# Optimization experiments

Measured on AMD Instinct MI355X. Metric: run time of the kernel, lower is better.

Reference implementation:

```python
import jax, jax.numpy as jnp
import numpy as np

N_NODES = 200000
N_EDGES = 3200000
NX = 8
NK = 2


def _l2norm(x, eps=1e-12):
    # F.normalize(x, p=2, dim=-1)
    n = jnp.linalg.norm(x, axis=-1, keepdims=True)
    return x / jnp.maximum(n, eps)


def _aniso_conv(x, src, dst, Kw, n_nodes):
    """For each kernel j: out_j[t] = sum_{e: dst[e]=t} Kw[j,e] * x[src[e]].
    Concatenate over kernels along the feature axis."""
    g = x[src]  # [E, d] gather
    def agg(w):  # w: [E]
        return jax.ops.segment_sum(w[:, None] * g, dst, num_segments=n_nodes)
    out = jax.vmap(agg)(Kw)  # [nk, N, d]
    return jnp.transpose(out, (1, 0, 2)).reshape(n_nodes, -1)  # [N, nk*d]


def setup_inputs() -> dict:
    key = jax.random.key(0)
    ks = jax.random.split(key, 8)
    x = jax.random.normal(ks[0], (N_NODES, NX), dtype=jnp.float32)
    src = jax.random.randint(ks[1], (N_EDGES,), 0, N_NODES, dtype=jnp.int64 if jax.config.jax_enable_x64 else jnp.int32)
    dst = jax.random.randint(ks[2], (N_EDGES,), 0, N_NODES, dtype=src.dtype)
    edge_index = jnp.stack([src, dst], axis=0)
    Kw = jax.random.normal(ks[3], (NK, N_EDGES), dtype=jnp.float32)
    d0, d1 = NX * NK, NX * NK * 2          # 16, 32
    d2 = d1 * NK                            # 64
    hidden, out_ch = 128, 64
    W0 = jax.random.normal(ks[4], (d0, d1), dtype=jnp.float32) / np.sqrt(d0)
    b0 = jnp.zeros((d1,), dtype=jnp.float32)
    W1 = jax.random.normal(ks[5], (d2, hidden), dtype=jnp.float32) / np.sqrt(d2)
    b1 = jnp.zeros((hidden,), dtype=jnp.float32)
    W2 = jax.random.normal(ks[6], (hidden, out_ch), dtype=jnp.float32) / np.sqrt(hidden)
    b2 = jnp.zeros((out_ch,), dtype=jnp.float32)
    return {"x": x, "edge_index": edge_index, "Kw": Kw,
            "W0": W0, "b0": b0, "W1": W1, "b1": b1, "W2": W2, "b2": b2}


def reference(x, edge_index, Kw, W0, b0, W1, b1, W2, b2):
    src, dst = edge_index[0], edge_index[1]
    n = x.shape[0]
    # layer 0: AnisoConv -> single-linear MLP -> L2 normalize
    h = _aniso_conv(x, src, dst, Kw, n)      # [N, 16]
    h = h @ W0 + b0                           # [N, 32]
    h = _l2norm(h)
    # layer 1: AnisoConv -> 2-layer MLP (ReLU between) -> L2 normalize
    h = _aniso_conv(h, src, dst, Kw, n)      # [N, 64]
    h = jax.nn.relu(h @ W1 + b1)             # [N, 128]
    h = h @ W2 + b2                           # [N, 64]
    h = _l2norm(h)
    return h
```

## Files before the change

kernel.cpp:

```cpp
#include <hip/hip_runtime.h>

#define NN 200000
#define NE 3200000
#define NB_SCAN 782
#define NBUCK 196
#define BSHIFT 10
#define BMASK 1023
#define SRCMASK 0x3FFFFu
#define NBLK_A 512
#define EPB (NE / NBLK_A)
#define NT_MLP1 12500

using bf16x8 = __attribute__((ext_vector_type(8))) short;
using f32x4  = __attribute__((ext_vector_type(4))) float;

__device__ __forceinline__ float bflo(unsigned u) { return __uint_as_float(u << 16); }
__device__ __forceinline__ float bfhi(unsigned u) { return __uint_as_float(u & 0xffff0000u); }
__device__ __forceinline__ unsigned short f2bfu(float f) {
  unsigned u = __float_as_uint(f);
  return (unsigned short)((u + 0x7fffu + ((u >> 16) & 1u)) >> 16);
}
__device__ __forceinline__ unsigned pack2(float a, float b) {
  return (unsigned)f2bfu(a) | ((unsigned)f2bfu(b) << 16);
}


__global__ __launch_bounds__(256) void bhist_kernel(const int* __restrict__ dst,
                                                    int* __restrict__ bhT) {
  __shared__ int h[NBUCK];
  for (int k = threadIdx.x; k < NBUCK; k += 256) h[k] = 0;
  __syncthreads();
  int base = blockIdx.x * EPB;
  for (int i = threadIdx.x; i < EPB; i += 256)
    atomicAdd(&h[dst[base + i] >> BSHIFT], 1);
  __syncthreads();
  for (int k = threadIdx.x; k < NBUCK; k += 256)
    bhT[k * NBLK_A + blockIdx.x] = h[k];
}

__global__ __launch_bounds__(NBLK_A) void bscan_kernel(int* __restrict__ bhT,
                                                       int* __restrict__ btot) {
  __shared__ int s[NBLK_A];
  int b = blockIdx.x;
  int v = bhT[b * NBLK_A + threadIdx.x];
  s[threadIdx.x] = v;
  __syncthreads();
#pragma unroll
  for (int off = 1; off < NBLK_A; off <<= 1) {
    int t = (threadIdx.x >= off) ? s[threadIdx.x - off] : 0;
    __syncthreads();
    s[threadIdx.x] += t;
    __syncthreads();
  }
  bhT[b * NBLK_A + threadIdx.x] = s[threadIdx.x] - v;
  if (threadIdx.x == NBLK_A - 1) btot[b] = s[NBLK_A - 1];
}

__global__ __launch_bounds__(256) void bbase_kernel(const int* __restrict__ btot,
                                                    int* __restrict__ bbase) {
  __shared__ int s[256];
  int v = (threadIdx.x < NBUCK) ? btot[threadIdx.x] : 0;
  s[threadIdx.x] = v;
  __syncthreads();
#pragma unroll
  for (int off = 1; off < 256; off <<= 1) {
    int t = (threadIdx.x >= off) ? s[threadIdx.x - off] : 0;
    __syncthreads();
    s[threadIdx.x] += t;
    __syncthreads();
  }
  if (threadIdx.x < NBUCK) bbase[threadIdx.x] = s[threadIdx.x] - v;
  if (threadIdx.x == NBUCK - 1) bbase[NBUCK] = s[threadIdx.x];
}

__global__ __launch_bounds__(256) void bplace_kernel(
    const int* __restrict__ src, const int* __restrict__ dst,
    const float* __restrict__ kw, const int* __restrict__ bhT,
    const int* __restrict__ bbase, uint2* __restrict__ bsorted) {
  __shared__ int cur[NBUCK];
  for (int k = threadIdx.x; k < NBUCK; k += 256)
    cur[k] = bbase[k] + bhT[k * NBLK_A + blockIdx.x];
  __syncthreads();
  int base = blockIdx.x * EPB;
  for (int i = threadIdx.x; i < EPB; i += 256) {
    int e = base + i;
    int d = dst[e];
    int p = atomicAdd(&cur[d >> BSHIFT], 1);
    uint2 u;
    u.x = (unsigned)src[e] | ((unsigned)(d & BMASK) << 18);
    u.y = pack2(kw[e], kw[NE + e]);
    bsorted[p] = u;
  }
}


__global__ __launch_bounds__(1024) void nhist_kernel(const uint2* __restrict__ bsorted,
                                                     const int* __restrict__ bbase,
                                                     int* __restrict__ cnt) {
  __shared__ int h[1024];
  h[threadIdx.x] = 0;
  __syncthreads();
  int b = blockIdx.x;
  int r0 = bbase[b], r1 = bbase[b + 1];
  for (int i = r0 + threadIdx.x; i < r1; i += 1024)
    atomicAdd(&h[bsorted[i].x >> 18], 1);
  __syncthreads();
  int node = b * 1024 + threadIdx.x;
  if (node < NN) cnt[node] = h[threadIdx.x];
}

__global__ __launch_bounds__(256) void scan1_kernel(const int* __restrict__ cnt,
                                                    int* __restrict__ offs,
                                                    int* __restrict__ bsums) {
  __shared__ int s[256];
  int i = blockIdx.x * 256 + threadIdx.x;
  int v = (i < NN) ? cnt[i] : 0;
  s[threadIdx.x] = v;
  __syncthreads();
#pragma unroll
  for (int off = 1; off < 256; off <<= 1) {
    int t = (threadIdx.x >= off) ? s[threadIdx.x - off] : 0;
    __syncthreads();
    s[threadIdx.x] += t;
    __syncthreads();
  }
  if (i < NN) offs[i] = s[threadIdx.x];
  if (threadIdx.x == 255) bsums[blockIdx.x] = s[255];
}

__global__ __launch_bounds__(1024) void scan2_kernel(int* __restrict__ bsums, int nb) {
  __shared__ int s[1024];
  int v = (threadIdx.x < nb) ? bsums[threadIdx.x] : 0;
  s[threadIdx.x] = v;
  __syncthreads();
#pragma unroll
  for (int off = 1; off < 1024; off <<= 1) {
    int t = (threadIdx.x >= off) ? s[threadIdx.x - off] : 0;
    __syncthreads();
    s[threadIdx.x] += t;
    __syncthreads();
  }
  if (threadIdx.x < nb) bsums[threadIdx.x] = s[threadIdx.x] - v;
}

__global__ __launch_bounds__(256) void scan3_kernel(const int* __restrict__ cnt,
                                                    const int* __restrict__ bsums,
                                                    int* __restrict__ offs) {
  int i = blockIdx.x * 256 + threadIdx.x;
  if (i >= NN) return;
  offs[i] = offs[i] - cnt[i] + bsums[blockIdx.x];
}

__global__ __launch_bounds__(1024) void nplace_kernel(const uint2* __restrict__ bsorted,
                                                      const int* __restrict__ bbase,
                                                      const int* __restrict__ offs,
                                                      uint2* __restrict__ sedge) {
  __shared__ int cur[1024];
  int b = blockIdx.x;
  int node = b * 1024 + threadIdx.x;
  cur[threadIdx.x] = (node < NN) ? offs[node] : 0;
  __syncthreads();
  int r0 = bbase[b], r1 = bbase[b + 1];
  for (int i = r0 + threadIdx.x; i < r1; i += 1024) {
    uint2 u = bsorted[i];
    int p = atomicAdd(&cur[u.x >> 18], 1);
    u.x &= SRCMASK;
    sedge[p] = u;
  }
}


__global__ __launch_bounds__(256) void fused0_kernel(
    const float* __restrict__ x, const int* __restrict__ offs,
    const int* __restrict__ cnt, const uint2* __restrict__ sedge,
    const float* __restrict__ W0, const float* __restrict__ b0,
    unsigned short* __restrict__ h1bf) {
  __shared__ float w0t[32][16];
  __shared__ float b0s[32];
  int tid = threadIdx.x;
  for (int i = tid; i < 16 * 32; i += 256) {
    int k = i >> 5, j = i & 31;
    w0t[j][k] = W0[i];
  }
  if (tid < 32) b0s[tid] = b0[tid];
  __syncthreads();

  int idx = blockIdx.x * 256 + tid;
  int node = idx >> 1, q = idx & 1;
  if (node >= NN) return;

  int start = offs[node];
  int deg = cnt[node];
  float a0 = 0.f, a1 = 0.f, a2 = 0.f, a3 = 0.f;
  float c0 = 0.f, c1 = 0.f, c2 = 0.f, c3 = 0.f;

  for (int i = 0; i < deg; ++i) {
    uint2 e = sedge[start + i];
    float k0 = bflo(e.y), k1 = bfhi(e.y);
    float4 v = *reinterpret_cast<const float4*>(x + (size_t)e.x * 8 + q * 4);
    a0 += k0 * v.x; a1 += k0 * v.y; a2 += k0 * v.z; a3 += k0 * v.w;
    c0 += k1 * v.x; c1 += k1 * v.y; c2 += k1 * v.z; c3 += k1 * v.w;
  }

  float pa0 = __shfl_xor(a0, 1), pa1 = __shfl_xor(a1, 1);
  float pa2 = __shfl_xor(a2, 1), pa3 = __shfl_xor(a3, 1);
  float pc0 = __shfl_xor(c0, 1), pc1 = __shfl_xor(c1, 1);
  float pc2 = __shfl_xor(c2, 1), pc3 = __shfl_xor(c3, 1);
  bool q0 = (q == 0);
  float h0 = q0 ? a0 : pa0, h1 = q0 ? a1 : pa1;
  float h2 = q0 ? a2 : pa2, h3 = q0 ? a3 : pa3;
  float h4 = q0 ? pa0 : a0, h5 = q0 ? pa1 : a1;
  float h6 = q0 ? pa2 : a2, h7 = q0 ? pa3 : a3;
  float h8 = q0 ? c0 : pc0, h9 = q0 ? c1 : pc1;
  float h10 = q0 ? c2 : pc2, h11 = q0 ? c3 : pc3;
  float h12 = q0 ? pc0 : c0, h13 = q0 ? pc1 : c1;
  float h14 = q0 ? pc2 : c2, h15 = q0 ? pc3 : c3;

  float o[16];
  float ss = 0.f;
#pragma unroll
  for (int jj = 0; jj < 16; ++jj) {
    int j = q * 16 + jj;
    float acc = b0s[j];
    acc += h0 * w0t[j][0] + h1 * w0t[j][1] + h2 * w0t[j][2] + h3 * w0t[j][3];
    acc += h4 * w0t[j][4] + h5 * w0t[j][5] + h6 * w0t[j][6] + h7 * w0t[j][7];
    acc += h8 * w0t[j][8] + h9 * w0t[j][9] + h10 * w0t[j][10] + h11 * w0t[j][11];
    acc += h12 * w0t[j][12] + h13 * w0t[j][13] + h14 * w0t[j][14] + h15 * w0t[j][15];
    o[jj] = acc;
    ss += acc * acc;
  }
  ss += __shfl_xor(ss, 1);
  float inv = 1.f / fmaxf(sqrtf(ss), 1e-12f);

  uint4* op = reinterpret_cast<uint4*>(h1bf + (size_t)node * 32 + q * 16);
  uint4 u0, u1;
  u0.x = pack2(o[0] * inv, o[1] * inv);  u0.y = pack2(o[2] * inv, o[3] * inv);
  u0.z = pack2(o[4] * inv, o[5] * inv);  u0.w = pack2(o[6] * inv, o[7] * inv);
  u1.x = pack2(o[8] * inv, o[9] * inv);  u1.y = pack2(o[10] * inv, o[11] * inv);
  u1.z = pack2(o[12] * inv, o[13] * inv); u1.w = pack2(o[14] * inv, o[15] * inv);
  op[0] = u0;
  op[1] = u1;
}


__global__ __launch_bounds__(256) void gather1_kernel(
    const unsigned short* __restrict__ h1bf, const int* __restrict__ offs,
    const int* __restrict__ cnt, const uint2* __restrict__ sedge,
    unsigned short* __restrict__ gbf) {
  int idx = blockIdx.x * 256 + threadIdx.x;
  int node = idx >> 2, q = idx & 3;
  if (node >= NN) return;
  int start = offs[node];
  int deg = cnt[node];

  float g0[8], g1[8];
#pragma unroll
  for (int k = 0; k < 8; ++k) { g0[k] = 0.f; g1[k] = 0.f; }

  for (int i = 0; i < deg; ++i) {
    uint2 e = sedge[start + i];
    float k0 = bflo(e.y), k1 = bfhi(e.y);
    uint4 u = *reinterpret_cast<const uint4*>(h1bf + (size_t)e.x * 32 + q * 8);
    float v0 = bflo(u.x), v1 = bfhi(u.x);
    float v2 = bflo(u.y), v3 = bfhi(u.y);
    float v4 = bflo(u.z), v5 = bfhi(u.z);
    float v6 = bflo(u.w), v7 = bfhi(u.w);
    g0[0] += k0 * v0; g0[1] += k0 * v1; g0[2] += k0 * v2; g0[3] += k0 * v3;
    g0[4] += k0 * v4; g0[5] += k0 * v5; g0[6] += k0 * v6; g0[7] += k0 * v7;
    g1[0] += k1 * v0; g1[1] += k1 * v1; g1[2] += k1 * v2; g1[3] += k1 * v3;
    g1[4] += k1 * v4; g1[5] += k1 * v5; g1[6] += k1 * v6; g1[7] += k1 * v7;
  }

  uint4 s0, s1;
  s0.x = pack2(g0[0], g0[1]); s0.y = pack2(g0[2], g0[3]);
  s0.z = pack2(g0[4], g0[5]); s0.w = pack2(g0[6], g0[7]);
  s1.x = pack2(g1[0], g1[1]); s1.y = pack2(g1[2], g1[3]);
  s1.z = pack2(g1[4], g1[5]); s1.w = pack2(g1[6], g1[7]);
  *reinterpret_cast<uint4*>(gbf + (size_t)node * 64 + q * 8) = s0;
  *reinterpret_cast<uint4*>(gbf + (size_t)node * 64 + 32 + q * 8) = s1;
}


__global__ __launch_bounds__(256) void mlp1_kernel(
    const unsigned short* __restrict__ gbf,
    const float* __restrict__ W1, const float* __restrict__ b1,
    const float* __restrict__ W2, const float* __restrict__ b2,
    float* __restrict__ out) {
  __shared__ __align__(16) short hlds[4][16][136];
  int tid = threadIdx.x;
  int wave = tid >> 6, lane = tid & 63;
  int lg = lane >> 4;
  int lr = lane & 15;

  bf16x8 w1f[8][2];
#pragma unroll
  for (int n = 0; n < 8; ++n)
#pragma unroll
    for (int ks = 0; ks < 2; ++ks) {
      bf16x8 f;
#pragma unroll
      for (int i = 0; i < 8; ++i)
        f[i] = (short)f2bfu(W1[(size_t)(ks * 32 + lg * 8 + i) * 128 + n * 16 + lr]);
      w1f[n][ks] = f;
    }
  bf16x8 w2f[4][4];
#pragma unroll
  for (int n2 = 0; n2 < 4; ++n2)
#pragma unroll
    for (int ks = 0; ks < 4; ++ks) {
      bf16x8 f;
#pragma unroll
      for (int i = 0; i < 8; ++i)
        f[i] = (short)f2bfu(W2[(size_t)(ks * 32 + lg * 8 + i) * 64 + n2 * 16 + lr]);
      w2f[n2][ks] = f;
    }
  float b1v[8], b2v[4];
#pragma unroll
  for (int n = 0; n < 8; ++n) b1v[n] = b1[n * 16 + lr];
#pragma unroll
  for (int n2 = 0; n2 < 4; ++n2) b2v[n2] = b2[n2 * 16 + lr];

  for (int tile = blockIdx.x * 4 + wave; tile < NT_MLP1; tile += gridDim.x * 4) {
    int base = tile * 16;
    const bf16x8* grow = reinterpret_cast<const bf16x8*>(gbf + (size_t)(base + lr) * 64);
    bf16x8 a1_0 = grow[lg];
    bf16x8 a1_1 = grow[4 + lg];

#pragma unroll
    for (int n = 0; n < 8; ++n) {
      f32x4 acc = {0.f, 0.f, 0.f, 0.f};
      acc = __builtin_amdgcn_mfma_f32_16x16x32_bf16(a1_0, w1f[n][0], acc, 0, 0, 0);
      acc = __builtin_amdgcn_mfma_f32_16x16x32_bf16(a1_1, w1f[n][1], acc, 0, 0, 0);
#pragma unroll
      for (int q = 0; q < 4; ++q) {
        float v = fmaxf(acc[q] + b1v[n], 0.f);
        hlds[wave][lg * 4 + q][n * 16 + lr] = (short)f2bfu(v);
      }
    }

    bf16x8 a2[4];
#pragma unroll
    for (int ks = 0; ks < 4; ++ks)
      a2[ks] = *reinterpret_cast<const bf16x8*>(&hlds[wave][lr][ks * 32 + lg * 8]);
    f32x4 acc2[4];
#pragma unroll
    for (int n2 = 0; n2 < 4; ++n2) {
      f32x4 a = {0.f, 0.f, 0.f, 0.f};
#pragma unroll
      for (int ks = 0; ks < 4; ++ks)
        a = __builtin_amdgcn_mfma_f32_16x16x32_bf16(a2[ks], w2f[n2][ks], a, 0, 0, 0);
      acc2[n2] = a;
    }

#pragma unroll
    for (int q = 0; q < 4; ++q) {
      float s = 0.f;
#pragma unroll
      for (int n2 = 0; n2 < 4; ++n2) {
        float v = acc2[n2][q] + b2v[n2];
        s += v * v;
      }
      s += __shfl_xor(s, 1); s += __shfl_xor(s, 2);
      s += __shfl_xor(s, 4); s += __shfl_xor(s, 8);
      float inv = 1.f / fmaxf(sqrtf(s), 1e-12f);
      size_t rowoff = (size_t)(base + lg * 4 + q) * 64 + lr;
#pragma unroll
      for (int n2 = 0; n2 < 4; ++n2)
        out[rowoff + n2 * 16] = (acc2[n2][q] + b2v[n2]) * inv;
    }
  }
}


extern "C" void kernel_launch(void* const* d_in, const int* in_sizes, int n_in,
                              void* d_out, int out_size, void* d_ws, size_t ws_size,
                              hipStream_t stream) {
  const float* x  = (const float*)d_in[0];
  const int* ei   = (const int*)d_in[1];
  const float* kw = (const float*)d_in[2];
  const float* W0 = (const float*)d_in[3];
  const float* b0 = (const float*)d_in[4];
  const float* W1 = (const float*)d_in[5];
  const float* b1 = (const float*)d_in[6];
  const float* W2 = (const float*)d_in[7];
  const float* b2 = (const float*)d_in[8];
  float* out = (float*)d_out;

  const int* src = ei;
  const int* dst = ei + NE;

  char* p = (char*)d_ws;
  uint2* bsorted = (uint2*)p;              p += (size_t)NE * 8;
  uint2* sedge   = (uint2*)p;              p += (size_t)NE * 8;
  unsigned short* h1bf = (unsigned short*)p; p += (size_t)NN * 32 * 2;
  int* bhT   = (int*)p;                    p += (size_t)NBUCK * NBLK_A * 4;
  int* btot  = (int*)p;                    p += (size_t)NBUCK * 4;
  int* bbase = (int*)p;                    p += (size_t)(NBUCK + 1) * 4;
  int* cnt   = (int*)p;                    p += (size_t)NN * 4;
  int* offs  = (int*)p;                    p += (size_t)NN * 4;
  int* bsums = (int*)p;                    p += 1024 * 4;
  unsigned short* gbf = (unsigned short*)bsorted;

  bhist_kernel<<<NBLK_A, 256, 0, stream>>>(dst, bhT);
  bscan_kernel<<<NBUCK, NBLK_A, 0, stream>>>(bhT, btot);
  bbase_kernel<<<1, 256, 0, stream>>>(btot, bbase);
  bplace_kernel<<<NBLK_A, 256, 0, stream>>>(src, dst, kw, bhT, bbase, bsorted);

  nhist_kernel<<<NBUCK, 1024, 0, stream>>>(bsorted, bbase, cnt);
  scan1_kernel<<<NB_SCAN, 256, 0, stream>>>(cnt, offs, bsums);
  scan2_kernel<<<1, 1024, 0, stream>>>(bsums, NB_SCAN);
  scan3_kernel<<<NB_SCAN, 256, 0, stream>>>(cnt, bsums, offs);
  nplace_kernel<<<NBUCK, 1024, 0, stream>>>(bsorted, bbase, offs, sedge);

  fused0_kernel<<<(2 * NN + 255) / 256, 256, 0, stream>>>(x, offs, cnt, sedge,
                                                          W0, b0, h1bf);
  gather1_kernel<<<(4 * NN + 255) / 256, 256, 0, stream>>>(h1bf, offs, cnt,
                                                           sedge, gbf);
  mlp1_kernel<<<768, 256, 0, stream>>>(gbf, W1, b1, W2, b2, out);
}
```

Before: 252.9 us.

## Sort edges by source within nodes, store x as bf16, one thread per node

nplace now keeps up to 18 edges per thread in registers and places them over 13 passes ordered by source-index range. Edges of each destination node therefore land roughly ordered by source, which should make the later gathers more cache-local. A new kernel converts x to bf16 so each gathered row is one 16-byte load, and fused0 moves to one thread per node, which removes the shuffle exchange. The cost is an extra kernel, reduced precision for the input features, and 13 block-wide syncs with higher register pressure in nplace.

After: 244.0 us. 3.5% less time.

```diff
diff --git a/kernel.cpp b/kernel.cpp
--- a/kernel.cpp
+++ b/kernel.cpp
@@ -10,6 +10,8 @@
 #define NBLK_A 512
 #define EPB (NE / NBLK_A)
 #define NT_MLP1 12500
+#define NPASS 13
+#define EMAX 18
 
 using bf16x8 = __attribute__((ext_vector_type(8))) short;
 using f32x4  = __attribute__((ext_vector_type(4))) float;
@@ -161,17 +163,54 @@
   cur[threadIdx.x] = (node < NN) ? offs[node] : 0;
   __syncthreads();
   int r0 = bbase[b], r1 = bbase[b + 1];
-  for (int i = r0 + threadIdx.x; i < r1; i += 1024) {
+  int i0 = r0 + threadIdx.x;
+
+  uint2 e[EMAX];
+#pragma unroll
+  for (int j = 0; j < EMAX; ++j) {
+    int i = i0 + j * 1024;
+    if (i < r1) e[j] = bsorted[i];
+  }
+
+  for (int p = 0; p < NPASS; ++p) {
+#pragma unroll
+    for (int j = 0; j < EMAX; ++j) {
+      int i = i0 + j * 1024;
+      if (i < r1) {
+        unsigned srcv = e[j].x & SRCMASK;
+        if ((int)(srcv >> 14) == p) {
+          int pos = atomicAdd(&cur[e[j].x >> 18], 1);
+          uint2 w; w.x = srcv; w.y = e[j].y;
+          sedge[pos] = w;
+        }
+      }
+    }
+    __syncthreads();
+  }
+  for (int i = i0 + EMAX * 1024; i < r1; i += 1024) {
     uint2 u = bsorted[i];
-    int p = atomicAdd(&cur[u.x >> 18], 1);
+    int pos = atomicAdd(&cur[u.x >> 18], 1);
     u.x &= SRCMASK;
-    sedge[p] = u;
-  }
+    sedge[pos] = u;
+  }
+}
+
+
+__global__ __launch_bounds__(256) void xcvt_kernel(const float* __restrict__ x,
+                                                   unsigned short* __restrict__ xbf) {
+  int i = blockIdx.x * 256 + threadIdx.x;
+  if (i >= NN) return;
+  const float4* xp = reinterpret_cast<const float4*>(x + (size_t)i * 8);
+  float4 a = xp[0], b = xp[1];
+  uint4 u;
+  u.x = pack2(a.x, a.y); u.y = pack2(a.z, a.w);
+  u.z = pack2(b.x, b.y); u.w = pack2(b.z, b.w);
+  *reinterpret_cast<uint4*>(xbf + (size_t)i * 8) = u;
 }
 
 
 __global__ __launch_bounds__(256) void fused0_kernel(
-    const float* __restrict__ x, const int* __restrict__ offs,
+    const unsigned short* __restrict__ xbf, const int* __restrict__ offs,
     const int* __restrict__ cnt, const uint2* __restrict__ sedge,
     const float* __restrict__ W0, const float* __restrict__ b0,
     unsigned short* __restrict__ h1bf) {
@@ -185,61 +224,50 @@
   if (tid < 32) b0s[tid] = b0[tid];
   __syncthreads();
 
-  int idx = blockIdx.x * 256 + tid;
-  int node = idx >> 1, q = idx & 1;
+  int node = blockIdx.x * 256 + tid;
   if (node >= NN) return;
 
   int start = offs[node];
   int deg = cnt[node];
-  float a0 = 0.f, a1 = 0.f, a2 = 0.f, a3 = 0.f;
-  float c0 = 0.f, c1 = 0.f, c2 = 0.f, c3 = 0.f;
+  float h16[16];
+#pragma unroll
+  for (int k = 0; k < 16; ++k) h16[k] = 0.f;
 
   for (int i = 0; i < deg; ++i) {
     uint2 e = sedge[start + i];
     float k0 = bflo(e.y), k1 = bfhi(e.y);
-    float4 v = *reinterpret_cast<const float4*>(x + (size_t)e.x * 8 + q * 4);
-    a0 += k0 * v.x; a1 += k0 * v.y; a2 += k0 * v.z; a3 += k0 * v.w;
-    c0 += k1 * v.x; c1 += k1 * v.y; c2 += k1 * v.z; c3 += k1 * v.w;
-  }
-
-  float pa0 = __shfl_xor(a0, 1), pa1 = __shfl_xor(a1, 1);
-  float pa2 = __shfl_xor(a2, 1), pa3 = __shfl_xor(a3, 1);
-  float pc0 = __shfl_xor(c0, 1), pc1 = __shfl_xor(c1, 1);
-  float pc2 = __shfl_xor(c2, 1), pc3 = __shfl_xor(c3, 1);
-  bool q0 = (q == 0);
-  float h0 = q0 ? a0 : pa0, h1 = q0 ? a1 : pa1;
-  float h2 = q0 ? a2 : pa2, h3 = q0 ? a3 : pa3;
-  float h4 = q0 ? pa0 : a0, h5 = q0 ? pa1 : a1;
-  float h6 = q0 ? pa2 : a2, h7 = q0 ? pa3 : a3;
-  float h8 = q0 ? c0 : pc0, h9 = q0 ? c1 : pc1;
-  float h10 = q0 ? c2 : pc2, h11 = q0 ? c3 : pc3;
-  float h12 = q0 ? pc0 : c0, h13 = q0 ? pc1 : c1;
-  float h14 = q0 ? pc2 : c2, h15 = q0 ? pc3 : c3;
-
-  float o[16];
+    uint4 u = *reinterpret_cast<const uint4*>(xbf + (size_t)e.x * 8);
+    float v0 = bflo(u.x), v1 = bfhi(u.x);
+    float v2 = bflo(u.y), v3 = bfhi(u.y);
+    float v4 = bflo(u.z), v5 = bfhi(u.z);
+    float v6 = bflo(u.w), v7 = bfhi(u.w);
+    h16[0] += k0 * v0; h16[1] += k0 * v1; h16[2] += k0 * v2; h16[3] += k0 * v3;
+    h16[4] += k0 * v4; h16[5] += k0 * v5; h16[6] += k0 * v6; h16[7] += k0 * v7;
+    h16[8]  += k1 * v0; h16[9]  += k1 * v1; h16[10] += k1 * v2; h16[11] += k1 * v3;
+    h16[12] += k1 * v4; h16[13] += k1 * v5; h16[14] += k1 * v6; h16[15] += k1 * v7;
+  }
+
+  float o[32];
   float ss = 0.f;
 #pragma unroll
-  for (int jj = 0; jj < 16; ++jj) {
-    int j = q * 16 + jj;
+  for (int j = 0; j < 32; ++j) {
     float acc = b0s[j];
-    acc += h0 * w0t[j][0] + h1 * w0t[j][1] + h2 * w0t[j][2] + h3 * w0t[j][3];
-    acc += h4 * w0t[j][4] + h5 * w0t[j][5] + h6 * w0t[j][6] + h7 * w0t[j][7];
-    acc += h8 * w0t[j][8] + h9 * w0t[j][9] + h10 * w0t[j][10] + h11 * w0t[j][11];
-    acc += h12 * w0t[j][12] + h13 * w0t[j][13] + h14 * w0t[j][14] + h15 * w0t[j][15];
-    o[jj] = acc;
+#pragma unroll
+    for (int k = 0; k < 16; ++k) acc += h16[k] * w0t[j][k];
+    o[j] = acc;
     ss += acc * acc;
   }
-  ss += __shfl_xor(ss, 1);
   float inv = 1.f / fmaxf(sqrtf(ss), 1e-12f);
-
-  uint4* op = reinterpret_cast<uint4*>(h1bf + (size_t)node * 32 + q * 16);
-  uint4 u0, u1;
-  u0.x = pack2(o[0] * inv, o[1] * inv);  u0.y = pack2(o[2] * inv, o[3] * inv);
-  u0.z = pack2(o[4] * inv, o[5] * inv);  u0.w = pack2(o[6] * inv, o[7] * inv);
-  u1.x = pack2(o[8] * inv, o[9] * inv);  u1.y = pack2(o[10] * inv, o[11] * inv);
-  u1.z = pack2(o[12] * inv, o[13] * inv); u1.w = pack2(o[14] * inv, o[15] * inv);
-  op[0] = u0;
-  op[1] = u1;
+  uint4* op = reinterpret_cast<uint4*>(h1bf + (size_t)node * 32);
+#pragma unroll
+  for (int c = 0; c < 4; ++c) {
+    uint4 u;
+    u.x = pack2(o[c * 8 + 0] * inv, o[c * 8 + 1] * inv);
+    u.y = pack2(o[c * 8 + 2] * inv, o[c * 8 + 3] * inv);
+    u.z = pack2(o[c * 8 + 4] * inv, o[c * 8 + 5] * inv);
+    u.w = pack2(o[c * 8 + 6] * inv, o[c * 8 + 7] * inv);
+    op[c] = u;
+  }
 }
 
 
@@ -393,6 +421,7 @@
   uint2* bsorted = (uint2*)p;              p += (size_t)NE * 8;
   uint2* sedge   = (uint2*)p;              p += (size_t)NE * 8;
   unsigned short* h1bf = (unsigned short*)p; p += (size_t)NN * 32 * 2;
+  unsigned short* xbf  = (unsigned short*)p; p += (size_t)NN * 8 * 2;
   int* bhT   = (int*)p;                    p += (size_t)NBUCK * NBLK_A * 4;
   int* btot  = (int*)p;                    p += (size_t)NBUCK * 4;
   int* bbase = (int*)p;                    p += (size_t)(NBUCK + 1) * 4;
@@ -401,6 +430,8 @@
   int* bsums = (int*)p;                    p += 1024 * 4;
   unsigned short* gbf = (unsigned short*)bsorted;
 
+  xcvt_kernel<<<NB_SCAN, 256, 0, stream>>>(x, xbf);
+
   bhist_kernel<<<NBLK_A, 256, 0, stream>>>(dst, bhT);
   bscan_kernel<<<NBUCK, NBLK_A, 0, stream>>>(bhT, btot);
   bbase_kernel<<<1, 256, 0, stream>>>(btot, bbase);
@@ -412,8 +443,7 @@
   scan3_kernel<<<NB_SCAN, 256, 0, stream>>>(cnt, bsums, offs);
   nplace_kernel<<<NBUCK, 1024, 0, stream>>>(bsorted, bbase, offs, sedge);
 
-  fused0_kernel<<<(2 * NN + 255) / 256, 256, 0, stream>>>(x, offs, cnt, sedge,
-                                                          W0, b0, h1bf);
+  fused0_kernel<<<NB_SCAN, 256, 0, stream>>>(xbf, offs, cnt, sedge, W0, b0, h1bf);
   gather1_kernel<<<(4 * NN + 255) / 256, 256, 0, stream>>>(h1bf, offs, cnt,
                                                            sedge, gbf);
   mlp1_kernel<<<768, 256, 0, stream>>>(gbf, W1, b1, W2, b2, out);
```
